# Optimization experiments

Measured on AMD Instinct MI355X. Metric: run time of the kernel, lower is better.

Reference implementation:

```python
import jax, jax.numpy as jnp
import numpy as np

C = 256
NUM_HEADS = 4
GROUPS = 8
EPS = 1e-5


def setup_inputs() -> dict:
    key = jax.random.key(0)
    ks = jax.random.split(key, 8)
    N, H, W = 4, 64, 64
    x = jax.random.normal(ks[0], (N, C, H, W), dtype=jnp.float32)
    mask = jnp.ones((N, 1, H, W), dtype=jnp.float32)
    norm_w = jax.random.normal(ks[1], (C,), dtype=jnp.float32) * 0.02 + 1.0
    norm_b = jax.random.normal(ks[2], (C,), dtype=jnp.float32) * 0.02
    qkv_w = jax.random.normal(ks[3], (3 * C, C), dtype=jnp.float32) * (1.0 / np.sqrt(C))
    qkv_b = jax.random.normal(ks[4], (3 * C,), dtype=jnp.float32) * 0.02
    proj_w = jax.random.normal(ks[5], (C, C), dtype=jnp.float32) * (1.0 / np.sqrt(C))
    proj_b = jax.random.normal(ks[6], (C,), dtype=jnp.float32) * 0.02
    return {"x": x, "mask": mask, "norm_w": norm_w, "norm_b": norm_b,
            "qkv_w": qkv_w, "qkv_b": qkv_b, "proj_w": proj_w, "proj_b": proj_b}


def _group_norm(x, w, b):
    # x: [N, C, H, W]; normalize within GROUPS groups over (C//G, H, W)
    N, Cc, H, W = x.shape
    xg = x.reshape(N, GROUPS, Cc // GROUPS, H, W)
    mean = xg.mean(axis=(2, 3, 4), keepdims=True)
    var = xg.var(axis=(2, 3, 4), keepdims=True)
    xg = (xg - mean) * jax.lax.rsqrt(var + EPS)
    x = xg.reshape(N, Cc, H, W)
    return x * w[None, :, None, None] + b[None, :, None, None]


def reference(x, mask, norm_w, norm_b, qkv_w, qkv_b, proj_w, proj_b):
    N, Cc, H, W = x.shape
    h = NUM_HEADS
    hd = Cc // h  # head dim
    x_norm = _group_norm(x, norm_w, norm_b)
    # 1x1 conv == channel matmul: [N, 3C, H, W]
    qkv = jnp.einsum('nchw,oc->nohw', x_norm, qkv_w) + qkv_b[None, :, None, None]
    q, k, v = jnp.split(qkv, 3, axis=1)
    # n (h c) y x -> n h (y x) c
    def to_heads(t):
        return t.reshape(N, h, hd, H * W).transpose(0, 1, 3, 2)
    q, k, v = to_heads(q), to_heads(k), to_heads(v)
    scale = hd ** (-0.5)
    scores = jnp.einsum('nhic,nhjc->nhij', q, k) * scale  # [N,h,HW,HW]
    probs = jax.nn.softmax(scores, axis=-1)
    out = jnp.einsum('nhij,nhjc->nhic', probs, v)  # [N,h,HW,hd]
    # n h (y x) c -> n (h c) y x
    out = out.transpose(0, 1, 3, 2).reshape(N, Cc, H, W)
    out = jnp.einsum('nchw,oc->nohw', out, proj_w) + proj_b[None, :, None, None]
    y = (x + out) * mask[:, :1, :, :]  # broadcast over C (== repeat)
    return (y, mask)
```

## Files before the change

kernel.cpp:

```cpp
#include <hip/hip_runtime.h>

#define HW 4096
#define EPSV 1e-5f
#define SCL (0.125f * 1.44269504088896341f)

typedef unsigned short u16;
typedef unsigned int u32;
typedef __attribute__((ext_vector_type(8))) short short8;
typedef __attribute__((ext_vector_type(4))) short short4v;
typedef __attribute__((ext_vector_type(4))) float f32x4;

#define MFMA_K32(a, b, c) __builtin_amdgcn_mfma_f32_16x16x32_bf16((a), (b), (c), 0, 0, 0)
#if __has_builtin(__builtin_amdgcn_mfma_f32_16x16x16bf16_1k)
#define MFMA_K16(a, b, c) __builtin_amdgcn_mfma_f32_16x16x16bf16_1k((a), (b), (c), 0, 0, 0)
#elif __has_builtin(__builtin_amdgcn_mfma_f32_16x16x16_bf16)
#define MFMA_K16(a, b, c) __builtin_amdgcn_mfma_f32_16x16x16_bf16((a), (b), (c), 0, 0, 0)
#else
#define MFMA_K16(a, b, c) (c)
#endif

#define GLDS(g, l) __builtin_amdgcn_global_load_lds( \
    (const __attribute__((address_space(1))) u16*)(g), \
    (__attribute__((address_space(3))) u16*)(l), 16, 0, 0)

__device__ __forceinline__ u16 f2b(float f) {
    u32 u = __float_as_uint(f);
    u32 r = (u + 0x7FFFu + ((u >> 16) & 1u)) >> 16;
    return (u16)r;
}

__global__ __launch_bounds__(256) void gn_wprep(const float* __restrict__ x, float* __restrict__ ps,
                                                const float* __restrict__ mask, float* __restrict__ outm,
                                                const float* __restrict__ qkv_w, u16* __restrict__ Wqb,
                                                const float* __restrict__ proj_w, u16* __restrict__ Wpb) {
    int bid = blockIdx.x;
    int t = threadIdx.x;
    if (bid < 16) {
        ((float4*)outm)[bid * 256 + t] = ((const float4*)mask)[bid * 256 + t];
    }
    if (bid < 256) {
        const float* src; u16* dst; int nscaled; int idx;
        if (bid < 192) { src = qkv_w; dst = Wqb; nscaled = 256; idx = bid * 256 + t; }
        else           { src = proj_w; dst = Wpb; nscaled = 0;   idx = (bid - 192) * 256 + t; }
        int row = idx >> 6;
        float sc = (row < nscaled) ? SCL : 1.0f;
        float4 v = *((const float4*)src + idx);
        u32 lo = (u32)f2b(v.x * sc) | ((u32)f2b(v.y * sc) << 16);
        u32 hi = (u32)f2b(v.z * sc) | ((u32)f2b(v.w * sc) << 16);
        uint2 o; o.x = lo; o.y = hi;
        *(uint2*)(dst + (size_t)idx * 4) = o;
    }
    const float4* base = (const float4*)x + (size_t)bid * 2048;
    float s = 0.f, sq = 0.f;
    for (int i = t; i < 2048; i += 256) {
        float4 v = base[i];
        s += v.x + v.y + v.z + v.w;
        sq += v.x * v.x + v.y * v.y + v.z * v.z + v.w * v.w;
    }
    __shared__ float rs[256], rq[256];
    rs[t] = s; rq[t] = sq;
    __syncthreads();
    for (int o = 128; o > 0; o >>= 1) {
        if (t < o) { rs[t] += rs[t + o]; rq[t] += rq[t + o]; }
        __syncthreads();
    }
    if (t == 0) { ps[2 * bid] = rs[0]; ps[2 * bid + 1] = rq[0]; }
}

__global__ __launch_bounds__(512) void qkv_fused(const float* __restrict__ x, const float* __restrict__ ps,
                                                 const float* __restrict__ nw, const float* __restrict__ nb,
                                                 const u16* __restrict__ Wb, const float* __restrict__ bq,
                                                 u16* __restrict__ Qw, u16* __restrict__ Kw, u16* __restrict__ Vw) {
    __shared__ u16 Xs[64 * 256];
    __shared__ u16 Tt[64][72];
    __shared__ float gm[8], gr[8];
    int t = threadIdx.x;
    int w = t >> 6, lane = t & 63;
    int hh = w >> 2, wl = w & 3;
    int col = lane & 15, quad = lane >> 4;
    int p0 = blockIdx.x * 64;
    int n = blockIdx.z;

    const u16* wrow = Wb + (size_t)(hh * 64 + wl * 16 + col) * 256 + quad * 8;
    short8 A[8];
#pragma unroll
    for (int ks = 0; ks < 8; ks++) A[ks] = *(const short8*)(wrow + ks * 32);

    if (t < 8) {
        float s = 0.f, sq = 0.f;
        for (int i = 0; i < 16; i++) {
            s += ps[2 * ((n * 8 + t) * 16 + i)];
            sq += ps[2 * ((n * 8 + t) * 16 + i) + 1];
        }
        float mean = s * (1.f / 131072.f);
        float var = sq * (1.f / 131072.f) - mean * mean;
        gm[t] = mean;
        gr[t] = rsqrtf(var + EPSV);
    }
    __syncthreads();

    int pc = (t & 15) * 4;
#pragma unroll
    for (int cb = 0; cb < 4; cb++) {
        int c0 = cb * 64;
#pragma unroll
        for (int jj = 0; jj < 2; jj++) {
            int r = (t >> 4) + jj * 32;
            int c = c0 + r;
            int g = c >> 5;
            float a = gr[g] * nw[c];
            float bb = nb[c] - gm[g] * a;
            float4 v = *(const float4*)(x + ((size_t)n * 256 + c) * HW + p0 + pc);
            Tt[pc + 0][r] = f2b(v.x * a + bb);
            Tt[pc + 1][r] = f2b(v.y * a + bb);
            Tt[pc + 2][r] = f2b(v.z * a + bb);
            Tt[pc + 3][r] = f2b(v.w * a + bb);
        }
        __syncthreads();
        int p = t >> 3, ck = t & 7;
        short8 s0 = *(const short8*)&Tt[p][ck * 8];
        int ch = cb * 8 + ck;
        *(short8*)(Xs + p * 256 + ((ch ^ (p & 7)) * 8)) = s0;
        __syncthreads();
    }

    int c7 = col & 7;
    for (int oi = 0; oi < 6; oi++) {
        int ot = oi * 2 + hh;
        int o0 = ot * 64;
        short8 An[8];
        if (oi < 5) {
            const u16* wn = wrow + (size_t)(oi + 1) * 128 * 256;
#pragma unroll
            for (int ks = 0; ks < 8; ks++) An[ks] = *(const short8*)(wn + ks * 32);
        }

        f32x4 C[4];
#pragma unroll
        for (int pb = 0; pb < 4; pb++) C[pb] = (f32x4){0.f, 0.f, 0.f, 0.f};
#pragma unroll
        for (int pb = 0; pb < 4; pb++) {
            const u16* xr = Xs + (pb * 16 + col) * 256;
#pragma unroll
            for (int ks = 0; ks < 8; ks++) {
                int slot = (ks * 4 + quad) ^ c7;
                short8 Bf = *(const short8*)(xr + slot * 8);
                C[pb] = MFMA_K32(A[ks], Bf, C[pb]);
            }
        }

        int type = o0 >> 8;
        int h = (o0 >> 6) & 3;
        int nh = n * 4 + h;
        float sc = (type == 0) ? SCL : 1.0f;
        if (type == 2) {
#pragma unroll
            for (int rg = 0; rg < 4; rg++) {
                int d = wl * 16 + quad * 4 + rg;
                float bias = bq[o0 + d];
                u16* vb = Vw + ((size_t)nh * 64 + d) * HW + p0 + col;
#pragma unroll
                for (int pb = 0; pb < 4; pb++)
                    vb[pb * 16] = f2b(C[pb][rg] + bias);
            }
        } else {
            u16* dst = (type == 0 ? Qw : Kw) + ((size_t)nh * HW + p0 + col) * 64 + wl * 16 + quad * 4;
            float b0 = sc * bq[o0 + wl * 16 + quad * 4 + 0];
            float b1 = sc * bq[o0 + wl * 16 + quad * 4 + 1];
            float b2 = sc * bq[o0 + wl * 16 + quad * 4 + 2];
            float b3 = sc * bq[o0 + wl * 16 + quad * 4 + 3];
#pragma unroll
            for (int pb = 0; pb < 4; pb++) {
                uint2 o;
                o.x = (u32)f2b(C[pb][0] + b0) | ((u32)f2b(C[pb][1] + b1) << 16);
                o.y = (u32)f2b(C[pb][2] + b2) | ((u32)f2b(C[pb][3] + b3) << 16);
                *(uint2*)(dst + (size_t)(pb * 16) * 64) = o;
            }
        }
#pragma unroll
        for (int ks = 0; ks < 8; ks++) A[ks] = An[ks];
    }
}

__global__ __launch_bounds__(512, 4) void flash_mfma(const u16* __restrict__ Qw, const u16* __restrict__ Kw,
                                                     const u16* __restrict__ Vw, u16* __restrict__ attnT) {
    __shared__ u16 Ks[4][64 * 64];
    __shared__ u16 Vts[4][64 * 64];
    int t = threadIdx.x;
    int w = t >> 6, lane = t & 63;
    int half = w >> 2, wl = w & 3;
    int col = lane & 15, quad = lane >> 4;
    int q0 = blockIdx.x * 128;
    int nh = blockIdx.y;

    const u16* qp = Qw + ((size_t)nh * HW + q0 + wl * 32 + col) * 64 + quad * 8;
    short8 qa0 = *(const short8*)qp;
    short8 qa1 = *(const short8*)(qp + 32);
    short8 qc0 = *(const short8*)(qp + 1024);
    short8 qc1 = *(const short8*)(qp + 1024 + 32);

    f32x4 OaA[4], OaB[4];
#pragma unroll
    for (int db = 0; db < 4; db++) {
        OaA[db] = (f32x4){0.f, 0.f, 0.f, 0.f};
        OaB[db] = (f32x4){0.f, 0.f, 0.f, 0.f};
    }
    float lacA = 0.f, lacB = 0.f;

    const u16* kbase = Kw + (size_t)nh * HW * 64;
    const u16* vbase = Vw + (size_t)nh * 64 * HW;
    int lrK = lane >> 3;
    int ccK = lane & 7;
    size_t kSrc = (size_t)(wl * 8 + lrK) * 64 + (ccK ^ lrK) * 8;
    int jbase = half * 2048;

#define STAGE(jt_, b_) do { \
        int j0_ = jbase + (jt_) * 64; \
        _Pragma("unroll") \
        for (int s_ = 0; s_ < 2; s_++) \
            GLDS(kbase + (size_t)j0_ * 64 + kSrc + (size_t)(s_ * 32) * 64, &Ks[half * 2 + (b_)][(wl * 8 + s_ * 32) * 64]); \
        _Pragma("unroll") \
        for (int s_ = 0; s_ < 2; s_++) { \
            int d_ = wl * 8 + s_ * 32 + lrK; \
            GLDS(vbase + (size_t)d_ * HW + j0_ + ((ccK ^ lrK) * 8), &Vts[half * 2 + (b_)][(wl * 8 + s_ * 32) * 64]); \
        } \
    } while (0)

    STAGE(0, 0);
    STAGE(1, 1);

    int c7 = col & 7;
    for (int jt = 0; jt < 32; jt++) {
        int cur = jt & 1;
        if (jt < 31) { asm volatile("s_waitcnt vmcnt(4)" ::: "memory"); }
        else         { asm volatile("s_waitcnt vmcnt(0)" ::: "memory"); }
        __builtin_amdgcn_s_barrier();

        const u16* KsC = Ks[half * 2 + cur];
        const u16* VtC = Vts[half * 2 + cur];

        f32x4 sA[4], sB[4];
        __builtin_amdgcn_s_setprio(1);
#pragma unroll
        for (int jb = 0; jb < 4; jb++) {
            const u16* kr = KsC + (jb * 16 + col) * 64;
            short8 ka0 = *(const short8*)(kr + ((quad ^ c7) * 8));
            short8 ka1 = *(const short8*)(kr + (((quad + 4) ^ c7) * 8));
            f32x4 a = (f32x4){0.f, 0.f, 0.f, 0.f};
            a = MFMA_K32(ka0, qa0, a);
            a = MFMA_K32(ka1, qa1, a);
            sA[jb] = a;
            f32x4 b = (f32x4){0.f, 0.f, 0.f, 0.f};
            b = MFMA_K32(ka0, qc0, b);
            b = MFMA_K32(ka1, qc1, b);
            sB[jb] = b;
        }
        __builtin_amdgcn_s_setprio(0);

        short4v ptA[4], ptB[4];
#pragma unroll
        for (int jb = 0; jb < 4; jb++) {
            float ea0 = __builtin_amdgcn_exp2f(sA[jb][0]);
            float ea1 = __builtin_amdgcn_exp2f(sA[jb][1]);
            float ea2 = __builtin_amdgcn_exp2f(sA[jb][2]);
            float ea3 = __builtin_amdgcn_exp2f(sA[jb][3]);
            float eb0 = __builtin_amdgcn_exp2f(sB[jb][0]);
            float eb1 = __builtin_amdgcn_exp2f(sB[jb][1]);
            float eb2 = __builtin_amdgcn_exp2f(sB[jb][2]);
            float eb3 = __builtin_amdgcn_exp2f(sB[jb][3]);
            lacA += (ea0 + ea1) + (ea2 + ea3);
            lacB += (eb0 + eb1) + (eb2 + eb3);
            uint2 pa2, pb2;
            asm("v_cvt_pk_bf16_f32 %0, %1, %2" : "=v"(pa2.x) : "v"(ea0), "v"(ea1));
            asm("v_cvt_pk_bf16_f32 %0, %1, %2" : "=v"(pa2.y) : "v"(ea2), "v"(ea3));
            asm("v_cvt_pk_bf16_f32 %0, %1, %2" : "=v"(pb2.x) : "v"(eb0), "v"(eb1));
            asm("v_cvt_pk_bf16_f32 %0, %1, %2" : "=v"(pb2.y) : "v"(eb2), "v"(eb3));
            ptA[jb] = __builtin_bit_cast(short4v, pa2);
            ptB[jb] = __builtin_bit_cast(short4v, pb2);
        }

        __builtin_amdgcn_s_setprio(1);
#pragma unroll
        for (int db = 0; db < 4; db++) {
            const u16* vr = VtC + (db * 16 + col) * 64;
#pragma unroll
            for (int jb = 0; jb < 4; jb++) {
                int ch = jb * 2 + (quad >> 1);
                short4v va = *(const short4v*)(vr + ((ch ^ c7) * 8) + (quad & 1) * 4);
                OaA[db] = MFMA_K16(va, ptA[jb], OaA[db]);
                OaB[db] = MFMA_K16(va, ptB[jb], OaB[db]);
            }
        }
        __builtin_amdgcn_s_setprio(0);

        __builtin_amdgcn_s_barrier();
        if (jt < 30) STAGE(jt + 2, cur);
    }
#undef STAGE

    lacA += __shfl_xor(lacA, 16);
    lacB += __shfl_xor(lacB, 16);
    lacA += __shfl_xor(lacA, 32);
    lacB += __shfl_xor(lacB, 32);

    float* mO = (float*)&Ks[0][0];
    float* mL = (float*)&Vts[0][0];
    int widx = wl * 64 + lane;
    if (half == 1) {
#pragma unroll
        for (int db = 0; db < 4; db++) {
#pragma unroll
            for (int rg = 0; rg < 4; rg++) {
                mO[(db * 8 + rg) * 256 + widx] = OaA[db][rg];
                mO[(db * 8 + 4 + rg) * 256 + widx] = OaB[db][rg];
            }
        }
        mL[widx] = lacA;
        mL[256 + widx] = lacB;
    }
    __syncthreads();
    if (half == 0) {
        float lA = lacA + mL[widx];
        float lB = lacB + mL[256 + widx];
        float rlA = 1.0f / lA, rlB = 1.0f / lB;
        u16* abA = attnT + ((size_t)(nh >> 2) * HW + q0 + wl * 32 + col) * 256 + (nh & 3) * 64 + quad * 4;
        u16* abB = abA + 16 * 256;
#pragma unroll
        for (int db = 0; db < 4; db++) {
            float a0 = OaA[db][0] + mO[(db * 8 + 0) * 256 + widx];
            float a1 = OaA[db][1] + mO[(db * 8 + 1) * 256 + widx];
            float a2 = OaA[db][2] + mO[(db * 8 + 2) * 256 + widx];
            float a3 = OaA[db][3] + mO[(db * 8 + 3) * 256 + widx];
            float b0 = OaB[db][0] + mO[(db * 8 + 4) * 256 + widx];
            float b1 = OaB[db][1] + mO[(db * 8 + 5) * 256 + widx];
            float b2 = OaB[db][2] + mO[(db * 8 + 6) * 256 + widx];
            float b3 = OaB[db][3] + mO[(db * 8 + 7) * 256 + widx];
            uint2 oA, oB;
            oA.x = (u32)f2b(a0 * rlA) | ((u32)f2b(a1 * rlA) << 16);
            oA.y = (u32)f2b(a2 * rlA) | ((u32)f2b(a3 * rlA) << 16);
            oB.x = (u32)f2b(b0 * rlB) | ((u32)f2b(b1 * rlB) << 16);
            oB.y = (u32)f2b(b2 * rlB) | ((u32)f2b(b3 * rlB) << 16);
            *(uint2*)(abA + db * 16) = oA;
            *(uint2*)(abB + db * 16) = oB;
        }
    }
}

__global__ __launch_bounds__(256) void proj_mfma(const u16* __restrict__ attnT, const u16* __restrict__ Wpb,
                                                 const float* __restrict__ bp, const float* __restrict__ x,
                                                 const float* __restrict__ mask, float* __restrict__ out) {
    __shared__ u16 Xs[64 * 256];
    int t = threadIdx.x;
    int w = t >> 6, lane = t & 63;
    int col = lane & 15, quad = lane >> 4;
    int p0 = blockIdx.x * 64;
    int o0 = blockIdx.y * 64;
    int n = blockIdx.z;

#pragma unroll
    for (int j = 0; j < 8; j++) {
        int rl = j * 2 + (lane >> 5);
        int row = w * 16 + rl;
        int slot = (lane & 31) ^ (rl & 7);
        GLDS(attnT + ((size_t)n * HW + p0 + row) * 256 + slot * 8, Xs + (w * 16 + j * 2) * 256);
    }

    const u16* wrow = Wpb + (size_t)(o0 + w * 16 + col) * 256 + quad * 8;
    short8 A[8];
#pragma unroll
    for (int ks = 0; ks < 8; ks++) A[ks] = *(const short8*)(wrow + ks * 32);

    __syncthreads();

    int c7 = col & 7;
    f32x4 C[4];
#pragma unroll
    for (int pb = 0; pb < 4; pb++) C[pb] = (f32x4){0.f, 0.f, 0.f, 0.f};
#pragma unroll
    for (int pb = 0; pb < 4; pb++) {
        const u16* xr = Xs + (pb * 16 + col) * 256;
#pragma unroll
        for (int ks = 0; ks < 8; ks++) {
            int slot = (ks * 4 + quad) ^ c7;
            short8 Bf = *(const short8*)(xr + slot * 8);
            C[pb] = MFMA_K32(A[ks], Bf, C[pb]);
        }
    }

#pragma unroll
    for (int rg = 0; rg < 4; rg++) {
        int o = o0 + w * 16 + quad * 4 + rg;
        float bias = bp[o];
        const float* xb = x + ((size_t)n * 256 + o) * HW + p0 + col;
        float* ob = out + ((size_t)n * 256 + o) * HW + p0 + col;
        const float* mb = mask + (size_t)n * HW + p0 + col;
#pragma unroll
        for (int pb = 0; pb < 4; pb++) {
            float mv = mb[pb * 16];
            ob[pb * 16] = (xb[pb * 16] + C[pb][rg] + bias) * mv;
        }
    }
}

extern "C" void kernel_launch(void* const* d_in, const int* in_sizes, int n_in,
                              void* d_out, int out_size, void* d_ws, size_t ws_size,
                              hipStream_t stream) {
    const float* x = (const float*)d_in[0];
    const float* mask = (const float*)d_in[1];
    const float* norm_w = (const float*)d_in[2];
    const float* norm_b = (const float*)d_in[3];
    const float* qkv_w = (const float*)d_in[4];
    const float* qkv_b = (const float*)d_in[5];
    const float* proj_w = (const float*)d_in[6];
    const float* proj_b = (const float*)d_in[7];
    float* out = (float*)d_out;

    float* ws = (float*)d_ws;
    float* pstats = ws + 64;
    u16* xt = (u16*)(ws + 2048);
    u16* Qw = xt + 4194304;
    u16* Kw = Qw + 4194304;
    u16* Vw = Kw + 4194304;
    u16* attnT = Vw + 4194304;
    u16* Wqb = attnT + 4194304;
    u16* Wpb = Wqb + 196608;

    gn_wprep<<<512, 256, 0, stream>>>(x, pstats, mask, out + 4194304, qkv_w, Wqb, proj_w, Wpb);
    qkv_fused<<<dim3(64, 1, 4), 512, 0, stream>>>(x, pstats, norm_w, norm_b, Wqb, qkv_b, Qw, Kw, Vw);
    flash_mfma<<<dim3(32, 16), 512, 0, stream>>>(Qw, Kw, Vw, attnT);
    proj_mfma<<<dim3(64, 4, 4), 256, 0, stream>>>(attnT, Wpb, proj_b, x, mask, out);
}
```

Baseline: 198.4 us.

## Split KV range four ways with each wave covering 64 query rows

New measurement: 471.4 us. +137.6%, slower.

```diff
diff --git a/kernel.cpp b/kernel.cpp
--- a/kernel.cpp
+++ b/kernel.cpp
@@ -184,45 +184,50 @@
 
 __global__ __launch_bounds__(512, 4) void flash_mfma(const u16* __restrict__ Qw, const u16* __restrict__ Kw,
                                                      const u16* __restrict__ Vw, u16* __restrict__ attnT) {
-    __shared__ u16 Ks[4][64 * 64];
-    __shared__ u16 Vts[4][64 * 64];
+    __shared__ u16 Ks[8][32 * 64];
+    __shared__ u16 Vts[8][64 * 32];
     int t = threadIdx.x;
     int w = t >> 6, lane = t & 63;
-    int half = w >> 2, wl = w & 3;
+    int qt = w >> 1, wq = w & 1;
     int col = lane & 15, quad = lane >> 4;
     int q0 = blockIdx.x * 128;
     int nh = blockIdx.y;
 
-    const u16* qp = Qw + ((size_t)nh * HW + q0 + wl * 32 + col) * 64 + quad * 8;
-    short8 qa0 = *(const short8*)qp;
-    short8 qa1 = *(const short8*)(qp + 32);
-    short8 qc0 = *(const short8*)(qp + 1024);
-    short8 qc1 = *(const short8*)(qp + 1024 + 32);
-
-    f32x4 OaA[4], OaB[4];
-#pragma unroll
-    for (int db = 0; db < 4; db++) {
-        OaA[db] = (f32x4){0.f, 0.f, 0.f, 0.f};
-        OaB[db] = (f32x4){0.f, 0.f, 0.f, 0.f};
-    }
-    float lacA = 0.f, lacB = 0.f;
+    const u16* qp = Qw + ((size_t)nh * HW + q0 + wq * 64 + col) * 64 + quad * 8;
+    short8 qf[4][2];
+#pragma unroll
+    for (int g = 0; g < 4; g++) {
+        qf[g][0] = *(const short8*)(qp + g * 1024);
+        qf[g][1] = *(const short8*)(qp + g * 1024 + 32);
+    }
+
+    f32x4 Oa[4][4];
+    float lac[4];
+#pragma unroll
+    for (int g = 0; g < 4; g++) {
+        lac[g] = 0.f;
+#pragma unroll
+        for (int db = 0; db < 4; db++) Oa[g][db] = (f32x4){0.f, 0.f, 0.f, 0.f};
+    }
 
     const u16* kbase = Kw + (size_t)nh * HW * 64;
     const u16* vbase = Vw + (size_t)nh * 64 * HW;
-    int lrK = lane >> 3;
-    int ccK = lane & 7;
-    size_t kSrc = (size_t)(wl * 8 + lrK) * 64 + (ccK ^ lrK) * 8;
-    int jbase = half * 2048;
+    int lrK = lane >> 3, ccK = lane & 7;
+    int lrV = lane >> 2, cV = lane & 3;
+    int vsw = (lrV >> 1) & 3;
+    int jbase = qt * 1024;
 
 #define STAGE(jt_, b_) do { \
-        int j0_ = jbase + (jt_) * 64; \
+        int j0_ = jbase + (jt_) * 32; \
         _Pragma("unroll") \
         for (int s_ = 0; s_ < 2; s_++) \
-            GLDS(kbase + (size_t)j0_ * 64 + kSrc + (size_t)(s_ * 32) * 64, &Ks[half * 2 + (b_)][(wl * 8 + s_ * 32) * 64]); \
+            GLDS(kbase + (size_t)(j0_ + wq * 8 + s_ * 16 + lrK) * 64 + (ccK ^ lrK) * 8, \
+                 &Ks[qt * 2 + (b_)][(wq * 8 + s_ * 16) * 64]); \
         _Pragma("unroll") \
         for (int s_ = 0; s_ < 2; s_++) { \
-            int d_ = wl * 8 + s_ * 32 + lrK; \
-            GLDS(vbase + (size_t)d_ * HW + j0_ + ((ccK ^ lrK) * 8), &Vts[half * 2 + (b_)][(wl * 8 + s_ * 32) * 64]); \
+            int d_ = wq * 16 + s_ * 32 + lrV; \
+            GLDS(vbase + (size_t)d_ * HW + j0_ + ((cV ^ vsw) * 8), \
+                 &Vts[qt * 2 + (b_)][(wq * 16 + s_ * 32) * 32]); \
         } \
     } while (0)
 
@@ -230,65 +235,60 @@
     STAGE(1, 1);
 
     int c7 = col & 7;
+    int cs2 = (col >> 1) & 3;
     for (int jt = 0; jt < 32; jt++) {
         int cur = jt & 1;
         if (jt < 31) { asm volatile("s_waitcnt vmcnt(4)" ::: "memory"); }
         else         { asm volatile("s_waitcnt vmcnt(0)" ::: "memory"); }
         __builtin_amdgcn_s_barrier();
 
-        const u16* KsC = Ks[half * 2 + cur];
-        const u16* VtC = Vts[half * 2 + cur];
-
-        f32x4 sA[4], sB[4];
+        const u16* KsC = Ks[qt * 2 + cur];
+        const u16* VtC = Vts[qt * 2 + cur];
+
+        f32x4 s[2][4];
         __builtin_amdgcn_s_setprio(1);
 #pragma unroll
-        for (int jb = 0; jb < 4; jb++) {
+        for (int jb = 0; jb < 2; jb++) {
             const u16* kr = KsC + (jb * 16 + col) * 64;
             short8 ka0 = *(const short8*)(kr + ((quad ^ c7) * 8));
             short8 ka1 = *(const short8*)(kr + (((quad + 4) ^ c7) * 8));
-            f32x4 a = (f32x4){0.f, 0.f, 0.f, 0.f};
-            a = MFMA_K32(ka0, qa0, a);
-            a = MFMA_K32(ka1, qa1, a);
-            sA[jb] = a;
-            f32x4 b = (f32x4){0.f, 0.f, 0.f, 0.f};
-            b = MFMA_K32(ka0, qc0, b);
-            b = MFMA_K32(ka1, qc1, b);
-            sB[jb] = b;
+#pragma unroll
+            for (int g = 0; g < 4; g++) {
+                f32x4 a = (f32x4){0.f, 0.f, 0.f, 0.f};
+                a = MFMA_K32(ka0, qf[g][0], a);
+                a = MFMA_K32(ka1, qf[g][1], a);
+                s[jb][g] = a;
+            }
         }
         __builtin_amdgcn_s_setprio(0);
 
-        short4v ptA[4], ptB[4];
-#pragma unroll
-        for (int jb = 0; jb < 4; jb++) {
-            float ea0 = __builtin_amdgcn_exp2f(sA[jb][0]);
-            float ea1 = __builtin_amdgcn_exp2f(sA[jb][1]);
-            float ea2 = __builtin_amdgcn_exp2f(sA[jb][2]);
-            float ea3 = __builtin_amdgcn_exp2f(sA[jb][3]);
-            float eb0 = __builtin_amdgcn_exp2f(sB[jb][0]);
-            float eb1 = __builtin_amdgcn_exp2f(sB[jb][1]);
-            float eb2 = __builtin_amdgcn_exp2f(sB[jb][2]);
-            float eb3 = __builtin_amdgcn_exp2f(sB[jb][3]);
-            lacA += (ea0 + ea1) + (ea2 + ea3);
-            lacB += (eb0 + eb1) + (eb2 + eb3);
-            uint2 pa2, pb2;
-            asm("v_cvt_pk_bf16_f32 %0, %1, %2" : "=v"(pa2.x) : "v"(ea0), "v"(ea1));
-            asm("v_cvt_pk_bf16_f32 %0, %1, %2" : "=v"(pa2.y) : "v"(ea2), "v"(ea3));
-            asm("v_cvt_pk_bf16_f32 %0, %1, %2" : "=v"(pb2.x) : "v"(eb0), "v"(eb1));
-            asm("v_cvt_pk_bf16_f32 %0, %1, %2" : "=v"(pb2.y) : "v"(eb2), "v"(eb3));
-            ptA[jb] = __builtin_bit_cast(short4v, pa2);
-            ptB[jb] = __builtin_bit_cast(short4v, pb2);
+        short4v pt[4][2];
+#pragma unroll
+        for (int jb = 0; jb < 2; jb++) {
+#pragma unroll
+            for (int g = 0; g < 4; g++) {
+                float e0 = __builtin_amdgcn_exp2f(s[jb][g][0]);
+                float e1 = __builtin_amdgcn_exp2f(s[jb][g][1]);
+                float e2 = __builtin_amdgcn_exp2f(s[jb][g][2]);
+                float e3 = __builtin_amdgcn_exp2f(s[jb][g][3]);
+                lac[g] += (e0 + e1) + (e2 + e3);
+                uint2 p2;
+                asm("v_cvt_pk_bf16_f32 %0, %1, %2" : "=v"(p2.x) : "v"(e0), "v"(e1));
+                asm("v_cvt_pk_bf16_f32 %0, %1, %2" : "=v"(p2.y) : "v"(e2), "v"(e3));
+                pt[g][jb] = __builtin_bit_cast(short4v, p2);
+            }
         }
 
         __builtin_amdgcn_s_setprio(1);
 #pragma unroll
         for (int db = 0; db < 4; db++) {
-            const u16* vr = VtC + (db * 16 + col) * 64;
-#pragma unroll
-            for (int jb = 0; jb < 4; jb++) {
-                int ch = jb * 2 + (quad >> 1);
-                short4v va = *(const short4v*)(vr + ((ch ^ c7) * 8) + (quad & 1) * 4);
-                OaA[db] = MFMA_K16(va, ptA[jb], OaA[db]);
-                OaB[db] = MFMA_K16(va, ptB[jb], OaB[db]);
+            const u16* vr = VtC + (db * 16 + col) * 32;
+#pragma unroll
+            for (int jb = 0; jb < 2; jb++) {
+                short4v va = *(const short4v*)(vr + (((jb * 2 + (quad >> 1)) ^ cs2) * 8) + (quad & 1) * 4);
+#pragma unroll
+                for (int g = 0; g < 4; g++)
+                    Oa[g][db] = MFMA_K16(va, pt[g][jb], Oa[g][db]);
             }
         }
         __builtin_amdgcn_s_setprio(0);
@@ -298,52 +298,57 @@
     }
 #undef STAGE
 
-    lacA += __shfl_xor(lacA, 16);
-    lacB += __shfl_xor(lacB, 16);
-    lacA += __shfl_xor(lacA, 32);
-    lacB += __shfl_xor(lacB, 32);
-
-    float* mO = (float*)&Ks[0][0];
-    float* mL = (float*)&Vts[0][0];
-    int widx = wl * 64 + lane;
-    if (half == 1) {
-#pragma unroll
-        for (int db = 0; db < 4; db++) {
-#pragma unroll
-            for (int rg = 0; rg < 4; rg++) {
-                mO[(db * 8 + rg) * 256 + widx] = OaA[db][rg];
-                mO[(db * 8 + 4 + rg) * 256 + widx] = OaB[db][rg];
-            }
-        }
-        mL[widx] = lacA;
-        mL[256 + widx] = lacB;
-    }
-    __syncthreads();
-    if (half == 0) {
-        float lA = lacA + mL[widx];
-        float lB = lacB + mL[256 + widx];
-        float rlA = 1.0f / lA, rlB = 1.0f / lB;
-        u16* abA = attnT + ((size_t)(nh >> 2) * HW + q0 + wl * 32 + col) * 256 + (nh & 3) * 64 + quad * 4;
-        u16* abB = abA + 16 * 256;
-#pragma unroll
-        for (int db = 0; db < 4; db++) {
-            float a0 = OaA[db][0] + mO[(db * 8 + 0) * 256 + widx];
-            float a1 = OaA[db][1] + mO[(db * 8 + 1) * 256 + widx];
-            float a2 = OaA[db][2] + mO[(db * 8 + 2) * 256 + widx];
-            float a3 = OaA[db][3] + mO[(db * 8 + 3) * 256 + widx];
-            float b0 = OaB[db][0] + mO[(db * 8 + 4) * 256 + widx];
-            float b1 = OaB[db][1] + mO[(db * 8 + 5) * 256 + widx];
-            float b2 = OaB[db][2] + mO[(db * 8 + 6) * 256 + widx];
-            float b3 = OaB[db][3] + mO[(db * 8 + 7) * 256 + widx];
-            uint2 oA, oB;
-            oA.x = (u32)f2b(a0 * rlA) | ((u32)f2b(a1 * rlA) << 16);
-            oA.y = (u32)f2b(a2 * rlA) | ((u32)f2b(a3 * rlA) << 16);
-            oB.x = (u32)f2b(b0 * rlB) | ((u32)f2b(b1 * rlB) << 16);
-            oB.y = (u32)f2b(b2 * rlB) | ((u32)f2b(b3 * rlB) << 16);
-            *(uint2*)(abA + db * 16) = oA;
-            *(uint2*)(abB + db * 16) = oB;
-        }
-    }
+#pragma unroll
+    for (int g = 0; g < 4; g++) {
+        lac[g] += __shfl_xor(lac[g], 16);
+        lac[g] += __shfl_xor(lac[g], 32);
+    }
+
+    float* fb0 = (float*)&Ks[0][0];
+    float* fb1 = (float*)&Vts[0][0];
+#define OIDX(g_, db_, rg_) ((((wq * 4 + (g_)) * 4 + (db_)) * 4 + (rg_)) * 64 + lane)
+#define WRITE_O(fb_) do { _Pragma("unroll") for (int g_ = 0; g_ < 4; g_++) \
+        _Pragma("unroll") for (int db_ = 0; db_ < 4; db_++) \
+        _Pragma("unroll") for (int rg_ = 0; rg_ < 4; rg_++) \
+            (fb_)[OIDX(g_, db_, rg_)] = Oa[g_][db_][rg_]; } while (0)
+#define ADD_O(fb_) do { _Pragma("unroll") for (int g_ = 0; g_ < 4; g_++) \
+        _Pragma("unroll") for (int db_ = 0; db_ < 4; db_++) \
+        _Pragma("unroll") for (int rg_ = 0; rg_ < 4; rg_++) \
+            Oa[g_][db_][rg_] += (fb_)[OIDX(g_, db_, rg_)]; } while (0)
+
+    if (qt == 1) WRITE_O(fb0);
+    if (qt == 3) WRITE_O(fb1);
+    __syncthreads();
+    if (qt == 0) ADD_O(fb0);
+    if (qt == 2) ADD_O(fb1);
+    __syncthreads();
+    if (qt == 2) WRITE_O(fb0);
+    if (qt != 0 && quad == 0) {
+#pragma unroll
+        for (int g = 0; g < 4; g++)
+            fb1[(qt - 1) * 128 + wq * 64 + g * 16 + col] = lac[g];
+    }
+    __syncthreads();
+    if (qt == 0) {
+        ADD_O(fb0);
+#pragma unroll
+        for (int g = 0; g < 4; g++) {
+            int row = wq * 64 + g * 16 + col;
+            float l = lac[g] + fb1[row] + fb1[128 + row] + fb1[256 + row];
+            float rl = 1.0f / l;
+            u16* ab = attnT + ((size_t)(nh >> 2) * HW + q0 + row) * 256 + (nh & 3) * 64 + quad * 4;
+#pragma unroll
+            for (int db = 0; db < 4; db++) {
+                uint2 o;
+                o.x = (u32)f2b(Oa[g][db][0] * rl) | ((u32)f2b(Oa[g][db][1] * rl) << 16);
+                o.y = (u32)f2b(Oa[g][db][2] * rl) | ((u32)f2b(Oa[g][db][3] * rl) << 16);
+                *(uint2*)(ab + db * 16) = o;
+            }
+        }
+    }
+#undef OIDX
+#undef WRITE_O
+#undef ADD_O
 }
 
 __global__ __launch_bounds__(256) void proj_mfma(const u16* __restrict__ attnT, const u16* __restrict__ Wpb,
```
